# Performance work log

Hardware: AMD Instinct MI355X
Metric: run time of the kernel (lower is better)

## Reference

```python
import jax, jax.numpy as jnp
import numpy as np

WS = 7   # window size
NH = 6   # num heads

def _ln(x, g, b, eps=1e-5):
    m = x.mean(-1, keepdims=True)
    v = jnp.var(x, axis=-1, keepdims=True)
    return (x - m) * jax.lax.rsqrt(v + eps) * g + b

def setup_inputs() -> dict:
    key = jax.random.key(0)
    ks = jax.random.split(key, 12)
    B, H, W, C = 32, 56, 56, 192
    hid = int(C * 2.0)
    def n(k, shape, s=0.02):
        return jax.random.normal(k, shape, jnp.float32) * s
    return {
        "x": jax.random.normal(ks[0], (B, H * W, C), jnp.float32),
        "H": H, "W": W,
        "ln1_g": jnp.ones((C,), jnp.float32), "ln1_b": jnp.zeros((C,), jnp.float32),
        "qkv_w": n(ks[1], (3 * C, C)), "qkv_b": jnp.zeros((3 * C,), jnp.float32),
        "proj_w": n(ks[2], (C, C)), "proj_b": jnp.zeros((C,), jnp.float32),
        "dw_w": n(ks[3], (C, 1, 3, 3)),          # depthwise 3x3, groups=C
        "pw_w": n(ks[4], (C, C)),                 # pointwise 1x1 conv (no bias)
        "gate_w": n(ks[5], (C, C)), "gate_b": jnp.zeros((C,), jnp.float32),
        "temp_w": n(ks[6], (C, C)), "temp_b": jnp.zeros((C,), jnp.float32),
        "spec_w": n(ks[7], (C, C)), "spec_b": jnp.zeros((C,), jnp.float32),
        "fuse_w": n(ks[8], (C, C)),                # fuse 1x1 conv (no bias)
        "ln2_g": jnp.ones((C,), jnp.float32), "ln2_b": jnp.zeros((C,), jnp.float32),
        "mlp1_w": n(ks[9], (hid, C)), "mlp1_b": jnp.zeros((hid,), jnp.float32),
        "mlp2_w": n(ks[10], (C, hid)), "mlp2_b": jnp.zeros((C,), jnp.float32),
    }

def reference(x, H, W, ln1_g, ln1_b, qkv_w, qkv_b, proj_w, proj_b, dw_w, pw_w,
              gate_w, gate_b, temp_w, temp_b, spec_w, spec_b, fuse_w,
              ln2_g, ln2_b, mlp1_w, mlp1_b, mlp2_w, mlp2_b):
    B, L, C = x.shape
    hd = C // NH
    scale = hd ** -0.5
    shortcut = x
    xn = _ln(x, ln1_g, ln1_b).reshape(B, H, W, C)
    # pad to multiple of window size (no-op when divisible)
    pad_b = (-H) % WS
    pad_r = (-W) % WS
    xp = jnp.pad(xn, ((0, 0), (0, pad_b), (0, pad_r), (0, 0)))
    Hp, Wp = H + pad_b, W + pad_r
    # window partition -> [B*nW, N, C]
    xw = xp.reshape(B, Hp // WS, WS, Wp // WS, WS, C).transpose(0, 1, 3, 2, 4, 5).reshape(-1, WS * WS, C)
    qkv = xw @ qkv_w.T + qkv_b
    q, k, v = [t.reshape(-1, WS * WS, NH, hd).transpose(0, 2, 1, 3) for t in jnp.split(qkv, 3, axis=-1)]
    attn = jax.nn.softmax(jnp.einsum('whnd,whmd->whnm', q * scale, k), axis=-1)
    aw = jnp.einsum('whnm,whmd->whnd', attn, v).transpose(0, 2, 1, 3).reshape(-1, WS * WS, C)
    aw = aw @ proj_w.T + proj_b
    # window reverse -> [B, Hp, Wp, C]
    xr = aw.reshape(B, Hp // WS, Wp // WS, WS, WS, C).transpose(0, 1, 3, 2, 4, 5).reshape(B, Hp, Wp, C)
    x_attn = xr[:, :H, :W, :].transpose(0, 3, 1, 2)     # [B,C,H,W]
    x_conv = xn.transpose(0, 3, 1, 2)                    # [B,C,H,W]
    # local_conv: depthwise 3x3 -> GELU -> pointwise 1x1
    ld = jax.lax.conv_general_dilated(x_conv, dw_w, (1, 1), 'SAME',
                                      feature_group_count=C,
                                      dimension_numbers=('NCHW', 'OIHW', 'NCHW'))
    ld = jnp.einsum('oc,bchw->bohw', pw_w, jax.nn.gelu(ld, approximate=False))
    # global gate: GAP -> linear -> sigmoid
    gate = jax.nn.sigmoid(x_conv.mean((2, 3)) @ gate_w.T + gate_b)[:, :, None, None]
    xf = x_attn + ld + x_conv * gate
    # spectral-temporal attention (outer product of two softmaxes, scale=2.0)
    a_t = jax.nn.softmax(jnp.einsum('oc,bcw->bow', temp_w, xf.mean(2)) + temp_b[None, :, None], axis=-1)
    a_s = jax.nn.softmax(jnp.einsum('oc,bch->boh', spec_w, xf.mean(3)) + spec_b[None, :, None], axis=-1)
    xf = xf * (a_s[:, :, :, None] * a_t[:, :, None, :]) * 2.0
    xf = jnp.einsum('oc,bchw->bohw', fuse_w, xf)         # fuse 1x1 conv
    x = shortcut + xf.transpose(0, 2, 3, 1).reshape(B, H * W, C)
    # MLP with pre-norm residual (1x1 conv expand == linear, then fc)
    h = _ln(x, ln2_g, ln2_b)
    h = jax.nn.gelu(h @ mlp1_w.T + mlp1_b, approximate=False)
    x = x + (h @ mlp2_w.T + mlp2_b)
    return x
```

## Files before the change

kernel.cpp:

```cpp
#include <hip/hip_runtime.h>
#include <hip/hip_bf16.h>

typedef __hip_bfloat16 bf16;

#define BB 32
#define HH 56
#define WW 56
#define CC 192
#define LL 3136
#define MM (BB*LL)
#define C3 576
#define HIDN 384
#define NHEAD 6
#define HD 32
#define NWIN 2048

typedef short short8 __attribute__((ext_vector_type(8)));
typedef float f32x4 __attribute__((ext_vector_type(4)));

__device__ __forceinline__ float us2f(unsigned short u) {
    union { unsigned int i; float f; } v; v.i = ((unsigned int)u) << 16; return v.f;
}
__device__ __forceinline__ float b2f(bf16 h) { return __bfloat162float(h); }
__device__ __forceinline__ bf16 f2b(float f) { return __float2bfloat16(f); }
__device__ __forceinline__ short f2bs(float f) { bf16 h = f2b(f); return *reinterpret_cast<short*>(&h); }
__device__ __forceinline__ float ldv(const bf16* p) { return b2f(*p); }
__device__ __forceinline__ float ldv(const float* p) { return *p; }
__device__ __forceinline__ void stv(bf16* p, float v) { *p = f2b(v); }
__device__ __forceinline__ void stv(float* p, float v) { *p = v; }
__device__ __forceinline__ float gelu_exact(float x) {
    return 0.5f * x * (1.0f + erff(x * 0.70710678118654752f));
}
__device__ __forceinline__ void async_lds16(const void* g, void* l) {
    __builtin_amdgcn_global_load_lds(
        (const __attribute__((address_space(1))) void*)g,
        (__attribute__((address_space(3))) void*)l, 16, 0, 0);
}

__global__ __launch_bounds__(256)
void cvt8_kernel(const float* __restrict__ s0, bf16* __restrict__ d0, int n0,
                 const float* __restrict__ s1, bf16* __restrict__ d1, int n1,
                 const float* __restrict__ s2, bf16* __restrict__ d2, int n2,
                 const float* __restrict__ s3, bf16* __restrict__ d3, int n3,
                 const float* __restrict__ s4, bf16* __restrict__ d4, int n4,
                 const float* __restrict__ s5, bf16* __restrict__ d5, int n5,
                 const float* __restrict__ s6, bf16* __restrict__ d6, int n6,
                 const float* __restrict__ s7, bf16* __restrict__ d7, int n7)
{
    int i = blockIdx.x * 256 + threadIdx.x;
    if (i < n0) { d0[i] = f2b(s0[i]); return; } i -= n0;
    if (i < n1) { d1[i] = f2b(s1[i]); return; } i -= n1;
    if (i < n2) { d2[i] = f2b(s2[i]); return; } i -= n2;
    if (i < n3) { d3[i] = f2b(s3[i]); return; } i -= n3;
    if (i < n4) { d4[i] = f2b(s4[i]); return; } i -= n4;
    if (i < n5) { d5[i] = f2b(s5[i]); return; } i -= n5;
    if (i < n6) { d6[i] = f2b(s6[i]); return; } i -= n6;
    if (i < n7) { d7[i] = f2b(s7[i]); }
}

template<typename IT>
__global__ __launch_bounds__(256)
void ln_kernel(const IT* __restrict__ in, const float* __restrict__ g,
               const float* __restrict__ bvec, bf16* __restrict__ out,
               bf16* __restrict__ xcopy)
{
    int wid = threadIdx.x >> 6, lane = threadIdx.x & 63;
    int row = blockIdx.x * 4 + wid;
    const IT* p = in + (size_t)row * CC;
    float x0 = ldv(p + lane);
    float x1 = ldv(p + lane + 64);
    float x2 = ldv(p + lane + 128);
    float s  = x0 + x1 + x2;
    float sq = x0*x0 + x1*x1 + x2*x2;
    #pragma unroll
    for (int o = 32; o > 0; o >>= 1) {
        s  += __shfl_xor(s,  o, 64);
        sq += __shfl_xor(sq, o, 64);
    }
    float mean = s * (1.0f / CC);
    float var  = sq * (1.0f / CC) - mean * mean;
    float inv  = rsqrtf(fmaxf(var, 0.0f) + 1e-5f);
    bf16* q = out + (size_t)row * CC;
    q[lane]       = f2b((x0 - mean) * inv * g[lane]       + bvec[lane]);
    q[lane + 64]  = f2b((x1 - mean) * inv * g[lane + 64]  + bvec[lane + 64]);
    q[lane + 128] = f2b((x2 - mean) * inv * g[lane + 128] + bvec[lane + 128]);
    if (xcopy) {
        bf16* xq = xcopy + (size_t)row * CC;
        xq[lane]       = f2b(x0);
        xq[lane + 64]  = f2b(x1);
        xq[lane + 128] = f2b(x2);
    }
}

template<int EPI, bool RESID, int NN, int KK, typename RT, typename OT>
__global__ __launch_bounds__(256)
void mfma_gemm(const bf16* __restrict__ A, const bf16* __restrict__ W,
               const float* __restrict__ bias, const RT* __restrict__ resid,
               OT* __restrict__ out,
               const bf16* __restrict__ xn2, const float* __restrict__ gate)
{
    __shared__ __align__(16) short As[128 * 64];
    __shared__ __align__(16) short Bs[64 * 64];
    const int t    = threadIdx.x;
    const int lane = t & 63;
    const int w    = t >> 6;
    const int nx   = gridDim.x;
    const int nwg  = gridDim.x * gridDim.y;
    int hw  = blockIdx.y * nx + blockIdx.x;
    int wid = (nwg & 7) ? hw : ((hw & 7) * (nwg >> 3) + (hw >> 3));
    const int m0   = (wid / nx) * 128;
    const int n0   = (wid % nx) * 64;
    const int lr   = lane & 15;
    const int lg   = lane >> 4;

    f32x4 acc[2][4];
    #pragma unroll
    for (int i = 0; i < 2; ++i)
        #pragma unroll
        for (int j = 0; j < 4; ++j)
            acc[i][j] = (f32x4){0.f, 0.f, 0.f, 0.f};

    for (int k0 = 0; k0 < KK; k0 += 64) {
        const bf16* Ab = A + (size_t)m0 * KK + k0;
        const bf16* Wb = W + (size_t)n0 * KK + k0;
        #pragma unroll
        for (int li = 0; li < 4; ++li) {
            int chunk = li * 256 + t;
            int r = chunk >> 3, c = chunk & 7;
            int cs = c ^ (r & 7);
            async_lds16(Ab + (size_t)r * KK + (cs << 3),
                        &As[(li * 256 + w * 64) << 3]);
        }
        #pragma unroll
        for (int li = 0; li < 2; ++li) {
            int chunk = li * 256 + t;
            int r = chunk >> 3, c = chunk & 7;
            int cs = c ^ (r & 7);
            async_lds16(Wb + (size_t)r * KK + (cs << 3),
                        &Bs[(li * 256 + w * 64) << 3]);
        }
        __syncthreads();
        #pragma unroll
        for (int kf = 0; kf < 2; ++kf) {
            short8 a_[2], b_[4];
            #pragma unroll
            for (int mi = 0; mi < 2; ++mi) {
                int row = (w << 5) + (mi << 4) + lr;
                a_[mi] = *reinterpret_cast<const short8*>(
                    &As[(row << 6) + ((((kf << 2) + lg) ^ (row & 7)) << 3)]);
            }
            #pragma unroll
            for (int ni = 0; ni < 4; ++ni) {
                int rn = (ni << 4) + lr;
                b_[ni] = *reinterpret_cast<const short8*>(
                    &Bs[(rn << 6) + ((((kf << 2) + lg) ^ (rn & 7)) << 3)]);
            }
            #pragma unroll
            for (int mi = 0; mi < 2; ++mi)
                #pragma unroll
                for (int ni = 0; ni < 4; ++ni)
                    acc[mi][ni] = __builtin_amdgcn_mfma_f32_16x16x32_bf16(
                        a_[mi], b_[ni], acc[mi][ni], 0, 0, 0);
        }
        __syncthreads();
    }

    #pragma unroll
    for (int mi = 0; mi < 2; ++mi) {
        #pragma unroll
        for (int ni = 0; ni < 4; ++ni) {
            int col = n0 + (ni << 4) + lr;
            float bv = bias ? bias[col] : 0.f;
            #pragma unroll
            for (int r = 0; r < 4; ++r) {
                int row = m0 + (w << 5) + (mi << 4) + (lg << 2) + r;
                float c = acc[mi][ni][r] + bv;
                if (EPI == 1) c = gelu_exact(c);
                if (EPI == 2) {
                    int bidx = row / LL;
                    c += ldv(resid + (size_t)row * NN + col)
                       + b2f(xn2[(size_t)row * NN + col]) * gate[bidx * CC + col];
                }
                if (RESID) c += ldv(resid + (size_t)row * NN + col);
                stv(out + (size_t)row * NN + col, c);
            }
        }
    }
}

__global__ __launch_bounds__(256)
void winattn_kernel(const bf16* __restrict__ qkv, bf16* __restrict__ aw)
{
    __shared__ __align__(16) short Ps[4][64 * 40];
    __shared__ __align__(16) short Vt[4][32 * 72];

    const int w  = threadIdx.x >> 6;
    const int t  = threadIdx.x & 63;
    const int p  = blockIdx.x * 4 + w;
    const int wi = p / 6;
    const int head = p - wi * 6;
    const int b  = wi >> 6;
    const int wr = wi & 63;
    const int wy = wr >> 3, wx = wr & 7;
    const int lc = t & 15;
    const int lg = t >> 4;
    const float scale = 0.1767766952966369f;
    const bf16* qbase = qkv + (size_t)b * LL * C3 + head * HD;
    short* ps = Ps[w];
    short* vt = Vt[w];

    #pragma unroll
    for (int e = t; e < 512; e += 64) {
        int r = e >> 4, c = 48 + (e & 15);
        vt[r * 72 + c] = 0;
    }
    for (int e = t; e < 196; e += 64) {
        int tok = e >> 2, part = e & 3;
        int iy = tok / 7, ix = tok - iy * 7;
        size_t l = (size_t)(wy * 7 + iy) * 56 + wx * 7 + ix;
        uint4 pv = *reinterpret_cast<const uint4*>(qbase + l * C3 + 384 + (part << 3));
        unsigned short uv[8];
        *reinterpret_cast<uint4*>(uv) = pv;
        #pragma unroll
        for (int jj = 0; jj < 8; ++jj)
            vt[((part << 3) + jj) * 72 + tok] = (short)uv[jj];
    }

    const short8 zero8 = {0, 0, 0, 0, 0, 0, 0, 0};
    short8 a_[4], b_[4];
    #pragma unroll
    for (int mi = 0; mi < 4; ++mi) {
        int tk = (mi << 4) + lc;
        a_[mi] = zero8;
        if (tk < 49) {
            int iy = tk / 7, ix = tk - iy * 7;
            size_t l = (size_t)(wy * 7 + iy) * 56 + wx * 7 + ix;
            a_[mi] = *reinterpret_cast<const short8*>(qbase + l * C3 + (lg << 3));
        }
    }
    #pragma unroll
    for (int ni = 0; ni < 4; ++ni) {
        int rn = (ni << 4) + lc;
        b_[ni] = zero8;
        if (rn < 49) {
            int iy = rn / 7, ix = rn - iy * 7;
            size_t l = (size_t)(wy * 7 + iy) * 56 + wx * 7 + ix;
            b_[ni] = *reinterpret_cast<const short8*>(qbase + l * C3 + 192 + (lg << 3));
        }
    }

    f32x4 acc[4][4];
    #pragma unroll
    for (int i = 0; i < 4; ++i)
        #pragma unroll
        for (int j = 0; j < 4; ++j)
            acc[i][j] = (f32x4){0.f, 0.f, 0.f, 0.f};
    #pragma unroll
    for (int mi = 0; mi < 4; ++mi)
        #pragma unroll
        for (int ni = 0; ni < 4; ++ni)
            acc[mi][ni] = __builtin_amdgcn_mfma_f32_16x16x32_bf16(
                a_[mi], b_[ni], acc[mi][ni], 0, 0, 0);

    float rinv[4][4];
    #pragma unroll
    for (int mi = 0; mi < 4; ++mi) {
        #pragma unroll
        for (int r = 0; r < 4; ++r) {
            float mx = -1e30f;
            #pragma unroll
            for (int ni = 0; ni < 4; ++ni) {
                float v = acc[mi][ni][r];
                if (ni == 3 && lc != 0) v = -1e30f;
                mx = fmaxf(mx, v);
            }
            mx = fmaxf(mx, __shfl_xor(mx, 1, 64));
            mx = fmaxf(mx, __shfl_xor(mx, 2, 64));
            mx = fmaxf(mx, __shfl_xor(mx, 4, 64));
            mx = fmaxf(mx, __shfl_xor(mx, 8, 64));
            float sm = 0.f;
            int row = (mi << 4) + (lg << 2) + r;
            #pragma unroll
            for (int ni = 0; ni < 4; ++ni) {
                float e = (ni == 3 && lc != 0) ? 0.f
                        : __expf(scale * (acc[mi][ni][r] - mx));
                ps[row * 40 + (ni << 4) + lc] = f2bs(e);
                sm += e;
            }
            sm += __shfl_xor(sm, 1, 64);
            sm += __shfl_xor(sm, 2, 64);
            sm += __shfl_xor(sm, 4, 64);
            sm += __shfl_xor(sm, 8, 64);
            rinv[mi][r] = 1.0f / sm;
        }
    }

    f32x4 o[4][2];
    #pragma unroll
    for (int i = 0; i < 4; ++i) {
        o[i][0] = (f32x4){0.f, 0.f, 0.f, 0.f};
        o[i][1] = (f32x4){0.f, 0.f, 0.f, 0.f};
    }
    #pragma unroll
    for (int kf = 0; kf < 2; ++kf) {
        short8 pa[4], vb[2];
        #pragma unroll
        for (int mi = 0; mi < 4; ++mi)
            pa[mi] = *reinterpret_cast<const short8*>(
                &ps[((mi << 4) + lc) * 40 + (kf << 5) + (lg << 3)]);
        #pragma unroll
        for (int n2 = 0; n2 < 2; ++n2)
            vb[n2] = *reinterpret_cast<const short8*>(
                &vt[((n2 << 4) + lc) * 72 + (kf << 5) + (lg << 3)]);
        #pragma unroll
        for (int mi = 0; mi < 4; ++mi)
            #pragma unroll
            for (int n2 = 0; n2 < 2; ++n2)
                o[mi][n2] = __builtin_amdgcn_mfma_f32_16x16x32_bf16(
                    pa[mi], vb[n2], o[mi][n2], 0, 0, 0);
    }

    #pragma unroll
    for (int mi = 0; mi < 4; ++mi) {
        #pragma unroll
        for (int r = 0; r < 4; ++r) {
            int row = (mi << 4) + (lg << 2) + r;
            float inv = rinv[mi][r];
            ps[row * 40 + lc]      = f2bs(o[mi][0][r] * inv);
            ps[row * 40 + 16 + lc] = f2bs(o[mi][1][r] * inv);
        }
    }
    for (int e = t; e < 196; e += 64) {
        int tok = e >> 2, part = e & 3;
        int iy = tok / 7, ix = tok - iy * 7;
        size_t l = (size_t)(wy * 7 + iy) * 56 + wx * 7 + ix;
        *reinterpret_cast<uint4*>(aw + ((size_t)b * LL + l) * CC + head * HD + (part << 3)) =
            *reinterpret_cast<const uint4*>(&ps[tok * 40 + (part << 3)]);
    }
}

__global__ __launch_bounds__(256)
void dwconv_kernel(const bf16* __restrict__ xn, const float* __restrict__ w,
                   bf16* __restrict__ out)
{
    __shared__ float wl[9 * 288];
    const int t = threadIdx.x;
    for (int i = t; i < CC * 9; i += 256) {
        int c = i / 9, k = i - c * 9;
        wl[k * 288 + (c >> 3) * 12 + (c & 7)] = w[i];
    }
    __syncthreads();
    int e = blockIdx.x * 256 + t;
    int cg = e % 24;
    int pix = e / 24;
    int w_ = pix % WW;
    int t2 = pix / WW;
    int h_ = t2 % HH;
    int b  = t2 / HH;
    float acc[8] = {0.f,0.f,0.f,0.f,0.f,0.f,0.f,0.f};
    const bf16* rowbase = xn + ((size_t)b * HH * WW) * CC + (size_t)cg * 8;
    #pragma unroll
    for (int ky = 0; ky < 3; ++ky) {
        int hy = h_ + ky - 1;
        if (hy < 0 || hy >= HH) continue;
        #pragma unroll
        for (int kx = 0; kx < 3; ++kx) {
            int wx_ = w_ + kx - 1;
            if (wx_ < 0 || wx_ >= WW) continue;
            int k = ky * 3 + kx;
            const float4* wp = reinterpret_cast<const float4*>(&wl[k * 288 + cg * 12]);
            float4 w0 = wp[0];
            float4 w1 = wp[1];
            unsigned short u[8];
            *reinterpret_cast<uint4*>(u) = *reinterpret_cast<const uint4*>(
                rowbase + ((size_t)hy * WW + wx_) * CC);
            acc[0] += us2f(u[0]) * w0.x;
            acc[1] += us2f(u[1]) * w0.y;
            acc[2] += us2f(u[2]) * w0.z;
            acc[3] += us2f(u[3]) * w0.w;
            acc[4] += us2f(u[4]) * w1.x;
            acc[5] += us2f(u[5]) * w1.y;
            acc[6] += us2f(u[6]) * w1.z;
            acc[7] += us2f(u[7]) * w1.w;
        }
    }
    bf16 o8[8];
    #pragma unroll
    for (int j = 0; j < 8; ++j) o8[j] = f2b(gelu_exact(acc[j]));
    *reinterpret_cast<uint4*>(out + (size_t)e * 8) = *reinterpret_cast<uint4*>(o8);
}

__global__ __launch_bounds__(192)
void colsum_kernel(const bf16* __restrict__ xn, float* __restrict__ colsum)
{
    int b = blockIdx.y, g = blockIdx.x, c = threadIdx.x;
    float acc = 0.f;
    int l0 = g * 196;
    for (int l = l0; l < l0 + 196; ++l)
        acc += b2f(xn[((size_t)b * LL + l) * CC + c]);
    atomicAdd(&colsum[b * CC + c], acc);
}

__global__ __launch_bounds__(192)
void gate_kernel(const float* __restrict__ colsum, const float* __restrict__ gw,
                 const float* __restrict__ gb, float* __restrict__ gate)
{
    __shared__ float cm[CC];
    int b = blockIdx.x, o = threadIdx.x;
    cm[o] = colsum[b * CC + o] * (1.0f / LL);
    __syncthreads();
    float acc = gb[o];
    for (int c = 0; c < CC; ++c) acc += gw[o * CC + c] * cm[c];
    gate[b * CC + o] = 1.0f / (1.0f + expf(-acc));
}

__global__ __launch_bounds__(256)
void means_kernel(const bf16* __restrict__ xf, bf16* __restrict__ mh,
                  bf16* __restrict__ mw)
{
    int e = blockIdx.x * 256 + threadIdx.x;
    const int NHALF = BB * WW * 24;
    if (e < NHALF) {
        int cg = e % 24, c0 = cg << 3;
        int w_ = (e / 24) % WW;
        int b  = e / (24 * WW);
        float s[8] = {0.f,0.f,0.f,0.f,0.f,0.f,0.f,0.f};
        const bf16* base = xf + ((size_t)b * HH * WW + w_) * CC + c0;
        for (int h_ = 0; h_ < HH; ++h_) {
            unsigned short u[8];
            *reinterpret_cast<uint4*>(u) = *reinterpret_cast<const uint4*>(base + (size_t)h_ * WW * CC);
            #pragma unroll
            for (int j = 0; j < 8; ++j) s[j] += us2f(u[j]);
        }
        bf16 o8[8];
        #pragma unroll
        for (int j = 0; j < 8; ++j) o8[j] = f2b(s[j] * (1.0f / HH));
        *reinterpret_cast<uint4*>(mh + ((size_t)b * WW + w_) * CC + c0) =
            *reinterpret_cast<uint4*>(o8);
    } else {
        e -= NHALF;
        int cg = e % 24, c0 = cg << 3;
        int h_ = (e / 24) % HH;
        int b  = e / (24 * HH);
        float s[8] = {0.f,0.f,0.f,0.f,0.f,0.f,0.f,0.f};
        const bf16* base = xf + ((size_t)b * HH + h_) * WW * CC + c0;
        for (int w_ = 0; w_ < WW; ++w_) {
            unsigned short u[8];
            *reinterpret_cast<uint4*>(u) = *reinterpret_cast<const uint4*>(base + (size_t)w_ * CC);
            #pragma unroll
            for (int j = 0; j < 8; ++j) s[j] += us2f(u[j]);
        }
        bf16 o8[8];
        #pragma unroll
        for (int j = 0; j < 8; ++j) o8[j] = f2b(s[j] * (1.0f / WW));
        *reinterpret_cast<uint4*>(mw + ((size_t)b * HH + h_) * CC + c0) =
            *reinterpret_cast<uint4*>(o8);
    }
}

__global__ __launch_bounds__(256)
void axmfma_kernel(const bf16* __restrict__ mh, const bf16* __restrict__ wt,
                   float* __restrict__ at,
                   const bf16* __restrict__ mw, const bf16* __restrict__ ws,
                   float* __restrict__ as_)
{
    const int b = blockIdx.x;
    const bf16* mean; const bf16* wmat; float* out;
    if (blockIdx.y == 0) { mean = mh; wmat = wt; out = at; }
    else                 { mean = mw; wmat = ws; out = as_; }
    const int w  = threadIdx.x >> 6;
    const int t  = threadIdx.x & 63;
    const int lc = t & 15, lg = t >> 4;
    const bf16* mb = mean + (size_t)b * 56 * CC;
    const short8 zero8 = {0, 0, 0, 0, 0, 0, 0, 0};

    f32x4 acc[3][4];
    #pragma unroll
    for (int i = 0; i < 3; ++i)
        #pragma unroll
        for (int j = 0; j < 4; ++j)
            acc[i][j] = (f32x4){0.f, 0.f, 0.f, 0.f};

    #pragma unroll
    for (int kf = 0; kf < 6; ++kf) {
        short8 a_[3], b_[4];
        #pragma unroll
        for (int mi = 0; mi < 3; ++mi) {
            int o = ((w * 3 + mi) << 4) + lc;
            a_[mi] = *reinterpret_cast<const short8*>(wmat + (size_t)o * CC + (kf << 5) + (lg << 3));
        }
        #pragma unroll
        for (int ni = 0; ni < 4; ++ni) {
            int pos = (ni << 4) + lc;
            b_[ni] = (pos < 56)
                ? *reinterpret_cast<const short8*>(mb + (size_t)pos * CC + (kf << 5) + (lg << 3))
                : zero8;
        }
        #pragma unroll
        for (int mi = 0; mi < 3; ++mi)
            #pragma unroll
            for (int ni = 0; ni < 4; ++ni)
                acc[mi][ni] = __builtin_amdgcn_mfma_f32_16x16x32_bf16(
                    a_[mi], b_[ni], acc[mi][ni], 0, 0, 0);
    }

    #pragma unroll
    for (int mi = 0; mi < 3; ++mi) {
        #pragma unroll
        for (int r = 0; r < 4; ++r) {
            float mx = -1e30f;
            #pragma unroll
            for (int ni = 0; ni < 4; ++ni) {
                float v = acc[mi][ni][r];
                if (ni == 3 && lc >= 8) v = -1e30f;
                mx = fmaxf(mx, v);
            }
            mx = fmaxf(mx, __shfl_xor(mx, 1, 64));
            mx = fmaxf(mx, __shfl_xor(mx, 2, 64));
            mx = fmaxf(mx, __shfl_xor(mx, 4, 64));
            mx = fmaxf(mx, __shfl_xor(mx, 8, 64));
            float e[4];
            float sm = 0.f;
            #pragma unroll
            for (int ni = 0; ni < 4; ++ni) {
                e[ni] = (ni == 3 && lc >= 8) ? 0.f : __expf(acc[mi][ni][r] - mx);
                sm += e[ni];
            }
            sm += __shfl_xor(sm, 1, 64);
            sm += __shfl_xor(sm, 2, 64);
            sm += __shfl_xor(sm, 4, 64);
            sm += __shfl_xor(sm, 8, 64);
            float inv = 1.0f / sm;
            int o = ((w * 3 + mi) << 4) + (lg << 2) + r;
            #pragma unroll
            for (int ni = 0; ni < 4; ++ni) {
                int pos = (ni << 4) + lc;
                if (pos < 56)
                    out[((size_t)b * 56 + pos) * CC + o] = e[ni] * inv;
            }
        }
    }
}

__global__ __launch_bounds__(256)
void modulate_kernel(const bf16* __restrict__ xf, const float* __restrict__ a_s,
                     const float* __restrict__ a_t, bf16* __restrict__ xf2)
{
    int e = blockIdx.x * 256 + threadIdx.x;
    int cg = e % 24, c0 = cg << 3;
    int pix = e / 24;
    int w_ = pix % WW;
    int t2 = pix / WW;
    int h_ = t2 % HH;
    int b  = t2 / HH;
    unsigned short u[8];
    size_t base = (size_t)e * 8;
    *reinterpret_cast<uint4*>(u) = *reinterpret_cast<const uint4*>(xf + base);
    const float4* sp = reinterpret_cast<const float4*>(a_s + ((size_t)b * 56 + h_) * CC + c0);
    const float4* tp = reinterpret_cast<const float4*>(a_t + ((size_t)b * 56 + w_) * CC + c0);
    float4 s0 = sp[0], s1 = sp[1];
    float4 t0 = tp[0], t1 = tp[1];
    float ss[8] = {s0.x, s0.y, s0.z, s0.w, s1.x, s1.y, s1.z, s1.w};
    float tt[8] = {t0.x, t0.y, t0.z, t0.w, t1.x, t1.y, t1.z, t1.w};
    bf16 o8[8];
    #pragma unroll
    for (int j = 0; j < 8; ++j)
        o8[j] = f2b(us2f(u[j]) * ss[j] * tt[j] * 2.0f);
    *reinterpret_cast<uint4*>(xf2 + base) = *reinterpret_cast<uint4*>(o8);
}

extern "C" void kernel_launch(void* const* d_in, const int* in_sizes, int n_in,
                              void* d_out, int out_size, void* d_ws, size_t ws_size,
                              hipStream_t stream)
{
    const float* x      = (const float*)d_in[0];
    const float* ln1_g  = (const float*)d_in[3];
    const float* ln1_b  = (const float*)d_in[4];
    const float* qkv_w  = (const float*)d_in[5];
    const float* qkv_b  = (const float*)d_in[6];
    const float* proj_w = (const float*)d_in[7];
    const float* proj_b = (const float*)d_in[8];
    const float* dw_w   = (const float*)d_in[9];
    const float* pw_w   = (const float*)d_in[10];
    const float* gate_w = (const float*)d_in[11];
    const float* gate_b = (const float*)d_in[12];
    const float* temp_w = (const float*)d_in[13];
    const float* spec_w = (const float*)d_in[15];
    const float* fuse_w = (const float*)d_in[17];
    const float* ln2_g  = (const float*)d_in[18];
    const float* ln2_b  = (const float*)d_in[19];
    const float* mlp1_w = (const float*)d_in[20];
    const float* mlp1_b = (const float*)d_in[21];
    const float* mlp2_w = (const float*)d_in[22];
    const float* mlp2_b = (const float*)d_in[23];
    float* out = (float*)d_out;

    const size_t SLOT = (size_t)MM * CC * sizeof(bf16);
    char* ws = (char*)d_ws;

    bf16* s_xn    = (bf16*)(ws);
    bf16* s_qkv   = (bf16*)(ws + SLOT);
    bf16* s_aw    = (bf16*)(ws + 4 * SLOT);
    bf16* s_xattn = (bf16*)(ws + SLOT);
    bf16* s_dwg   = (bf16*)(ws + 2 * SLOT);
    bf16* s_xf    = (bf16*)(ws + 4 * SLOT);
    bf16* s_xf2   = (bf16*)(ws + 3 * SLOT);
    bf16* s_x2    = (bf16*)(ws);
    bf16* s_hn    = (bf16*)(ws + 2 * SLOT);
    bf16* s_h1    = (bf16*)(ws + 3 * SLOT);

    float* colsum  = (float*)(ws + 5 * SLOT);
    float* gatebuf = colsum + BB * CC;
    bf16*  mean_h  = (bf16*)(gatebuf + BB * CC);
    bf16*  mean_w  = mean_h + (size_t)BB * 56 * CC;
    float* a_t     = (float*)(mean_w + (size_t)BB * 56 * CC);
    float* a_s     = a_t + (size_t)BB * CC * 56;
    bf16* wb_qkv  = (bf16*)(a_s + (size_t)BB * CC * 56);
    bf16* wb_proj = wb_qkv  + C3 * CC;
    bf16* wb_pw   = wb_proj + CC * CC;
    bf16* wb_fuse = wb_pw   + CC * CC;
    bf16* wb_mlp1 = wb_fuse + CC * CC;
    bf16* wb_mlp2 = wb_mlp1 + HIDN * CC;
    bf16* wb_temp = wb_mlp2 + CC * HIDN;
    bf16* wb_spec = wb_temp + CC * CC;
    char* after_w = (char*)(wb_spec + CC * CC);
    size_t total_need = after_w - ws;
    if (ws_size < total_need) return;
    bf16* s_xb = (bf16*)after_w;
    bool have_xb = (ws_size >= total_need + SLOT);

    const int VEC_BLOCKS = MM * 24 / 256;
    const int CVT_N0 = C3 * CC, CVT_N1 = CC * CC, CVT_N4 = HIDN * CC;
    const int CVT_TOTAL = CVT_N0 + 5 * CVT_N1 + 2 * CVT_N4;

    cvt8_kernel<<<(CVT_TOTAL + 255) / 256, 256, 0, stream>>>(
        qkv_w, wb_qkv, CVT_N0, proj_w, wb_proj, CVT_N1, pw_w, wb_pw, CVT_N1,
        fuse_w, wb_fuse, CVT_N1, mlp1_w, wb_mlp1, CVT_N4, mlp2_w, wb_mlp2, CVT_N4,
        temp_w, wb_temp, CVT_N1, spec_w, wb_spec, CVT_N1);

    ln_kernel<float><<<MM / 4, 256, 0, stream>>>(x, ln1_g, ln1_b, s_xn,
                                                 have_xb ? s_xb : nullptr);
    mfma_gemm<0, false, C3, CC, bf16, bf16><<<dim3(C3 / 64, MM / 128), 256, 0, stream>>>(
        s_xn, wb_qkv, qkv_b, (const bf16*)nullptr, s_qkv, nullptr, nullptr);
    winattn_kernel<<<NWIN * NHEAD / 4, 256, 0, stream>>>(s_qkv, s_aw);
    mfma_gemm<0, false, CC, CC, bf16, bf16><<<dim3(CC / 64, MM / 128), 256, 0, stream>>>(
        s_aw, wb_proj, proj_b, (const bf16*)nullptr, s_xattn, nullptr, nullptr);
    dwconv_kernel<<<VEC_BLOCKS, 256, 0, stream>>>(s_xn, dw_w, s_dwg);
    hipMemsetAsync(colsum, 0, BB * CC * sizeof(float), stream);
    colsum_kernel<<<dim3(16, BB), 192, 0, stream>>>(s_xn, colsum);
    gate_kernel<<<BB, 192, 0, stream>>>(colsum, gate_w, gate_b, gatebuf);
    mfma_gemm<2, false, CC, CC, bf16, bf16><<<dim3(CC / 64, MM / 128), 256, 0, stream>>>(
        s_dwg, wb_pw, (const float*)nullptr, s_xattn, s_xf, s_xn, gatebuf);
    means_kernel<<<(2 * BB * WW * 24) / 256, 256, 0, stream>>>(s_xf, mean_h, mean_w);
    axmfma_kernel<<<dim3(BB, 2), 256, 0, stream>>>(
        mean_h, wb_temp, a_t, mean_w, wb_spec, a_s);
    modulate_kernel<<<VEC_BLOCKS, 256, 0, stream>>>(s_xf, a_s, a_t, s_xf2);
    if (have_xb)
        mfma_gemm<0, true, CC, CC, bf16, bf16><<<dim3(CC / 64, MM / 128), 256, 0, stream>>>(
            s_xf2, wb_fuse, (const float*)nullptr, s_xb, s_x2, nullptr, nullptr);
    else
        mfma_gemm<0, true, CC, CC, float, bf16><<<dim3(CC / 64, MM / 128), 256, 0, stream>>>(
            s_xf2, wb_fuse, (const float*)nullptr, x, s_x2, nullptr, nullptr);
    ln_kernel<bf16><<<MM / 4, 256, 0, stream>>>(s_x2, ln2_g, ln2_b, s_hn, nullptr);
    mfma_gemm<1, false, HIDN, CC, bf16, bf16><<<dim3(HIDN / 64, MM / 128), 256, 0, stream>>>(
        s_hn, wb_mlp1, mlp1_b, (const bf16*)nullptr, s_h1, nullptr, nullptr);
    mfma_gemm<0, true, CC, HIDN, bf16, float><<<dim3(CC / 64, MM / 128), 256, 0, stream>>>(
        s_h1, wb_mlp2, mlp2_b, s_x2, out, nullptr, nullptr);
}
```

Measured before the change: 391.7 us.

## Compute transposed scores in window attention and feed probabilities to PV via shuffles

Window attention now computes S^T = K·Q^T so each lane's accumulator column holds one query token. Softmax then reduces mostly in registers with only two cross-lane shuffles, and the probabilities are repacked into MFMA B operands with lane shuffles instead of a round trip through LDS. V is stored in a single XOR-swizzled LDS buffer that is reused for the output staging, which reduces LDS footprint and bank conflicts. This adds shuffle and select instructions and depends on the swizzle and lane mapping being correct.

After: 374.6 us. 1.05x faster.

```diff
diff --git a/kernel.cpp b/kernel.cpp
--- a/kernel.cpp
+++ b/kernel.cpp
@@ -24,6 +24,9 @@
 __device__ __forceinline__ float b2f(bf16 h) { return __bfloat162float(h); }
 __device__ __forceinline__ bf16 f2b(float f) { return __float2bfloat16(f); }
 __device__ __forceinline__ short f2bs(float f) { bf16 h = f2b(f); return *reinterpret_cast<short*>(&h); }
+__device__ __forceinline__ unsigned pk2(float a, float b) {
+    return (unsigned)(unsigned short)f2bs(a) | ((unsigned)(unsigned short)f2bs(b) << 16);
+}
 __device__ __forceinline__ float ldv(const bf16* p) { return b2f(*p); }
 __device__ __forceinline__ float ldv(const float* p) { return *p; }
 __device__ __forceinline__ void stv(bf16* p, float v) { *p = f2b(v); }
@@ -191,8 +194,7 @@
 __global__ __launch_bounds__(256)
 void winattn_kernel(const bf16* __restrict__ qkv, bf16* __restrict__ aw)
 {
-    __shared__ __align__(16) short Ps[4][64 * 40];
-    __shared__ __align__(16) short Vt[4][32 * 72];
+    __shared__ __align__(16) short Buf[4][2560];
 
     const int w  = threadIdx.x >> 6;
     const int t  = threadIdx.x & 63;
@@ -206,13 +208,12 @@
     const int lg = t >> 4;
     const float scale = 0.1767766952966369f;
     const bf16* qbase = qkv + (size_t)b * LL * C3 + head * HD;
-    short* ps = Ps[w];
-    short* vt = Vt[w];
+    short* buf = Buf[w];
 
     #pragma unroll
     for (int e = t; e < 512; e += 64) {
-        int r = e >> 4, c = 48 + (e & 15);
-        vt[r * 72 + c] = 0;
+        int d = e >> 4, k = 48 + (e & 15);
+        buf[(d << 6) + (((k >> 3) ^ (d & 7)) << 3) + (k & 7)] = 0;
     }
     for (int e = t; e < 196; e += 64) {
         int tok = e >> 2, part = e & 3;
@@ -222,30 +223,32 @@
         unsigned short uv[8];
         *reinterpret_cast<uint4*>(uv) = pv;
         #pragma unroll
-        for (int jj = 0; jj < 8; ++jj)
-            vt[((part << 3) + jj) * 72 + tok] = (short)uv[jj];
+        for (int jj = 0; jj < 8; ++jj) {
+            int d = (part << 3) + jj;
+            buf[(d << 6) + (((tok >> 3) ^ (d & 7)) << 3) + (tok & 7)] = (short)uv[jj];
+        }
     }
 
     const short8 zero8 = {0, 0, 0, 0, 0, 0, 0, 0};
-    short8 a_[4], b_[4];
+    short8 ka[4], qb[4];
     #pragma unroll
     for (int mi = 0; mi < 4; ++mi) {
-        int tk = (mi << 4) + lc;
-        a_[mi] = zero8;
-        if (tk < 49) {
-            int iy = tk / 7, ix = tk - iy * 7;
+        int key = (mi << 4) + lc;
+        ka[mi] = zero8;
+        if (key < 49) {
+            int iy = key / 7, ix = key - iy * 7;
             size_t l = (size_t)(wy * 7 + iy) * 56 + wx * 7 + ix;
-            a_[mi] = *reinterpret_cast<const short8*>(qbase + l * C3 + (lg << 3));
-        }
-    }
-    #pragma unroll
-    for (int ni = 0; ni < 4; ++ni) {
-        int rn = (ni << 4) + lc;
-        b_[ni] = zero8;
-        if (rn < 49) {
-            int iy = rn / 7, ix = rn - iy * 7;
+            ka[mi] = *reinterpret_cast<const short8*>(qbase + l * C3 + 192 + (lg << 3));
+        }
+    }
+    #pragma unroll
+    for (int nj = 0; nj < 4; ++nj) {
+        int tok = (nj << 4) + lc;
+        qb[nj] = zero8;
+        if (tok < 49) {
+            int iy = tok / 7, ix = tok - iy * 7;
             size_t l = (size_t)(wy * 7 + iy) * 56 + wx * 7 + ix;
-            b_[ni] = *reinterpret_cast<const short8*>(qbase + l * C3 + 192 + (lg << 3));
+            qb[nj] = *reinterpret_cast<const short8*>(qbase + l * C3 + (lg << 3));
         }
     }
 
@@ -258,84 +261,97 @@
     #pragma unroll
     for (int mi = 0; mi < 4; ++mi)
         #pragma unroll
-        for (int ni = 0; ni < 4; ++ni)
-            acc[mi][ni] = __builtin_amdgcn_mfma_f32_16x16x32_bf16(
-                a_[mi], b_[ni], acc[mi][ni], 0, 0, 0);
-
-    float rinv[4][4];
-    #pragma unroll
-    for (int mi = 0; mi < 4; ++mi) {
-        #pragma unroll
-        for (int r = 0; r < 4; ++r) {
-            float mx = -1e30f;
-            #pragma unroll
-            for (int ni = 0; ni < 4; ++ni) {
-                float v = acc[mi][ni][r];
-                if (ni == 3 && lc != 0) v = -1e30f;
-                mx = fmaxf(mx, v);
-            }
-            mx = fmaxf(mx, __shfl_xor(mx, 1, 64));
-            mx = fmaxf(mx, __shfl_xor(mx, 2, 64));
-            mx = fmaxf(mx, __shfl_xor(mx, 4, 64));
-            mx = fmaxf(mx, __shfl_xor(mx, 8, 64));
-            float sm = 0.f;
-            int row = (mi << 4) + (lg << 2) + r;
-            #pragma unroll
-            for (int ni = 0; ni < 4; ++ni) {
-                float e = (ni == 3 && lc != 0) ? 0.f
-                        : __expf(scale * (acc[mi][ni][r] - mx));
-                ps[row * 40 + (ni << 4) + lc] = f2bs(e);
+        for (int nj = 0; nj < 4; ++nj)
+            acc[mi][nj] = __builtin_amdgcn_mfma_f32_16x16x32_bf16(
+                ka[mi], qb[nj], acc[mi][nj], 0, 0, 0);
+
+    float rinv[4];
+    #pragma unroll
+    for (int nj = 0; nj < 4; ++nj) {
+        float mx = acc[0][nj][0];
+        #pragma unroll
+        for (int mi = 0; mi < 3; ++mi)
+            #pragma unroll
+            for (int r = 0; r < 4; ++r)
+                mx = fmaxf(mx, acc[mi][nj][r]);
+        float v48 = (lg == 0) ? acc[3][nj][0] : -1e30f;
+        mx = fmaxf(mx, v48);
+        mx = fmaxf(mx, __shfl_xor(mx, 16, 64));
+        mx = fmaxf(mx, __shfl_xor(mx, 32, 64));
+        float sm = 0.f;
+        #pragma unroll
+        for (int mi = 0; mi < 3; ++mi)
+            #pragma unroll
+            for (int r = 0; r < 4; ++r) {
+                float e = __expf(scale * (acc[mi][nj][r] - mx));
+                acc[mi][nj][r] = e;
                 sm += e;
             }
-            sm += __shfl_xor(sm, 1, 64);
-            sm += __shfl_xor(sm, 2, 64);
-            sm += __shfl_xor(sm, 4, 64);
-            sm += __shfl_xor(sm, 8, 64);
-            rinv[mi][r] = 1.0f / sm;
-        }
-    }
-
-    f32x4 o[4][2];
-    #pragma unroll
-    for (int i = 0; i < 4; ++i) {
-        o[i][0] = (f32x4){0.f, 0.f, 0.f, 0.f};
-        o[i][1] = (f32x4){0.f, 0.f, 0.f, 0.f};
-    }
+        float e48 = (lg == 0) ? __expf(scale * (acc[3][nj][0] - mx)) : 0.f;
+        acc[3][nj][0] = e48; sm += e48;
+        acc[3][nj][1] = 0.f; acc[3][nj][2] = 0.f; acc[3][nj][3] = 0.f;
+        sm += __shfl_xor(sm, 16, 64);
+        sm += __shfl_xor(sm, 32, 64);
+        rinv[nj] = 1.0f / sm;
+    }
+
+    f32x4 acc2[2][4];
+    #pragma unroll
+    for (int i = 0; i < 2; ++i)
+        #pragma unroll
+        for (int j = 0; j < 4; ++j)
+            acc2[i][j] = (f32x4){0.f, 0.f, 0.f, 0.f};
+    const int src0 = ((lg & 1) << 5) + lc;
+    const int src1 = src0 + 16;
+    const bool hi = (lg >> 1) != 0;
     #pragma unroll
     for (int kf = 0; kf < 2; ++kf) {
-        short8 pa[4], vb[2];
-        #pragma unroll
-        for (int mi = 0; mi < 4; ++mi)
-            pa[mi] = *reinterpret_cast<const short8*>(
-                &ps[((mi << 4) + lc) * 40 + (kf << 5) + (lg << 3)]);
-        #pragma unroll
-        for (int n2 = 0; n2 < 2; ++n2)
-            vb[n2] = *reinterpret_cast<const short8*>(
-                &vt[((n2 << 4) + lc) * 72 + (kf << 5) + (lg << 3)]);
-        #pragma unroll
-        for (int mi = 0; mi < 4; ++mi)
-            #pragma unroll
-            for (int n2 = 0; n2 < 2; ++n2)
-                o[mi][n2] = __builtin_amdgcn_mfma_f32_16x16x32_bf16(
-                    pa[mi], vb[n2], o[mi][n2], 0, 0, 0);
-    }
-
-    #pragma unroll
-    for (int mi = 0; mi < 4; ++mi) {
-        #pragma unroll
-        for (int r = 0; r < 4; ++r) {
-            int row = (mi << 4) + (lg << 2) + r;
-            float inv = rinv[mi][r];
-            ps[row * 40 + lc]      = f2bs(o[mi][0][r] * inv);
-            ps[row * 40 + 16 + lc] = f2bs(o[mi][1][r] * inv);
-        }
-    }
+        short8 av[2];
+        #pragma unroll
+        for (int mi2 = 0; mi2 < 2; ++mi2) {
+            int d = (mi2 << 4) + lc;
+            av[mi2] = *reinterpret_cast<const short8*>(
+                &buf[(d << 6) + ((((kf << 2) + lg) ^ (d & 7)) << 3)]);
+        }
+        #pragma unroll
+        for (int nj = 0; nj < 4; ++nj) {
+            unsigned A0 = pk2(acc[2*kf][nj][0],   acc[2*kf][nj][1]);
+            unsigned A1 = pk2(acc[2*kf][nj][2],   acc[2*kf][nj][3]);
+            unsigned B0 = pk2(acc[2*kf+1][nj][0], acc[2*kf+1][nj][1]);
+            unsigned B1 = pk2(acc[2*kf+1][nj][2], acc[2*kf+1][nj][3]);
+            unsigned xa0 = __shfl(A0, src0, 64), xa1 = __shfl(A1, src0, 64);
+            unsigned xa2 = __shfl(A0, src1, 64), xa3 = __shfl(A1, src1, 64);
+            unsigned xb0 = __shfl(B0, src0, 64), xb1 = __shfl(B1, src0, 64);
+            unsigned xb2 = __shfl(B0, src1, 64), xb3 = __shfl(B1, src1, 64);
+            union { unsigned u[4]; short8 s; } ub;
+            ub.u[0] = hi ? xb0 : xa0;
+            ub.u[1] = hi ? xb1 : xa1;
+            ub.u[2] = hi ? xb2 : xa2;
+            ub.u[3] = hi ? xb3 : xa3;
+            #pragma unroll
+            for (int mi2 = 0; mi2 < 2; ++mi2)
+                acc2[mi2][nj] = __builtin_amdgcn_mfma_f32_16x16x32_bf16(
+                    av[mi2], ub.s, acc2[mi2][nj], 0, 0, 0);
+        }
+    }
+
+    #pragma unroll
+    for (int mi2 = 0; mi2 < 2; ++mi2)
+        #pragma unroll
+        for (int nj = 0; nj < 4; ++nj) {
+            int tokrow = (nj << 4) + lc;
+            #pragma unroll
+            for (int r = 0; r < 4; ++r) {
+                int d = (mi2 << 4) + (lg << 2) + r;
+                buf[tokrow * 40 + d] = f2bs(acc2[mi2][nj][r] * rinv[nj]);
+            }
+        }
     for (int e = t; e < 196; e += 64) {
         int tok = e >> 2, part = e & 3;
         int iy = tok / 7, ix = tok - iy * 7;
         size_t l = (size_t)(wy * 7 + iy) * 56 + wx * 7 + ix;
         *reinterpret_cast<uint4*>(aw + ((size_t)b * LL + l) * CC + head * HD + (part << 3)) =
-            *reinterpret_cast<const uint4*>(&ps[tok * 40 + (part << 3)]);
+            *reinterpret_cast<const uint4*>(&buf[tok * 40 + (part << 3)]);
     }
 }
 
```
